# Kernel optimization log

Hardware: AMD Instinct MI355X
Metric: run time of the kernel (lower is better)

The kernel has to match this reference:

```python
import jax, jax.numpy as jnp
import numpy as np

EPS = 1e-5

def _bn(x, g, b):
    # BatchNorm1d in training mode: stats over (batch, length) dims, biased var
    mean = jnp.mean(x, axis=(0, 2), keepdims=True)
    var = jnp.var(x, axis=(0, 2), keepdims=True)
    return (x - mean) * jax.lax.rsqrt(var + EPS) * g[None, :, None] + b[None, :, None]

def _conv1x1(x, w, b):
    # pointwise Conv1d: [B,C,T] x [O,C] -> [B,O,T]
    return jnp.einsum('bct,oc->bot', x, w) + b[None, :, None]

def setup_inputs() -> dict:
    key = jax.random.key(0)
    ks = jax.random.split(key, 4)
    B, C, T = 32, 1024, 2048
    x = jax.random.normal(ks[0], (B, C, T), dtype=jnp.float32)
    w1 = jax.random.normal(ks[1], (256, 1024), dtype=jnp.float32) * (1.0 / np.sqrt(1024))
    w2 = jax.random.normal(ks[2], (64, 256), dtype=jnp.float32) * (1.0 / np.sqrt(256))
    return {
        'x': x,
        'bn1_g': jnp.ones((1024,), jnp.float32), 'bn1_b': jnp.zeros((1024,), jnp.float32),
        'w1': w1, 'b1': jnp.zeros((256,), jnp.float32),
        'bn2_g': jnp.ones((256,), jnp.float32), 'bn2_b': jnp.zeros((256,), jnp.float32),
        'w2': w2, 'b2': jnp.zeros((64,), jnp.float32),
    }

def reference(x, bn1_g, bn1_b, w1, b1, bn2_g, bn2_b, w2, b2):
    # reduction layer: BN -> 1x1 conv -> ReLU (1024 -> 256)
    h = jax.nn.relu(_conv1x1(_bn(x, bn1_g, bn1_b), w1, b1))
    # out layer: BN -> 1x1 conv, no activation (256 -> 64)
    out = _conv1x1(_bn(h, bn2_g, bn2_b), w2, b2)
    o = out.shape[1]
    mu = out[:, : o // 2, :]
    logvar = out[:, o // 2 :, :]
    return (mu, logvar)
```

## Files before the change

kernel.cpp:

```cpp
#include <hip/hip_runtime.h>

#define B_  32
#define C1  1024
#define C2  256
#define T_  2048
#define EPSF 1e-5f
#define BPITCH 40

typedef __attribute__((ext_vector_type(8))) short bf16x8;
typedef __attribute__((ext_vector_type(4))) float f32x4;

static __device__ __forceinline__ unsigned short f2bf(float f) {
    union { float f; unsigned u; } v; v.f = f;
    unsigned r = v.u + 0x7fffu + ((v.u >> 16) & 1u);
    return (unsigned short)(r >> 16);
}
static __device__ __forceinline__ void g2l16(const void* g, void* l) {
    __builtin_amdgcn_global_load_lds(
        (const __attribute__((address_space(1))) unsigned int*)g,
        (__attribute__((address_space(3))) unsigned int*)l, 16, 0, 0);
}

__global__ __launch_bounds__(256) void k_stats(const float* __restrict__ x,
        float* __restrict__ psum, float* __restrict__ psq) {
    int ct = blockIdx.x, b = blockIdx.y, tid = threadIdx.x;
    int c0 = ct * 64;
    int cl = tid >> 2, t4 = tid & 3;
    const float* xrow = x + (size_t)b * C1 * T_ + (size_t)(c0 + cl) * T_ + t4 * 4;
    float s = 0.f, sq = 0.f;
    #pragma unroll 4
    for (int t0 = 0; t0 < T_; t0 += 16) {
        float4 v = *(const float4*)(xrow + t0);
        s  += v.x + v.y + v.z + v.w;
        sq += v.x * v.x + v.y * v.y + v.z * v.z + v.w * v.w;
    }
    s  += __shfl_xor(s, 1);  s  += __shfl_xor(s, 2);
    sq += __shfl_xor(sq, 1); sq += __shfl_xor(sq, 2);
    if (t4 == 0) {
        psum[(size_t)b * C1 + c0 + cl] = s;
        psq [(size_t)b * C1 + c0 + cl] = sq;
    }
}

__global__ __launch_bounds__(256) void k_bnstat1(const float* __restrict__ psum,
        const float* __restrict__ psq, const float* __restrict__ g1,
        const float* __restrict__ bb1, float* __restrict__ sc1, float* __restrict__ sh1) {
    int c = blockIdx.x * 256 + threadIdx.x;
    float s = 0.f, q = 0.f;
    for (int b = 0; b < B_; ++b) {
        s += psum[(size_t)b * C1 + c];
        q += psq[(size_t)b * C1 + c];
    }
    const float n = (float)(B_ * T_);
    float m = s / n;
    float sc = g1[c] * rsqrtf(q / n - m * m + EPSF);
    sc1[c] = sc;
    sh1[c] = bb1[c] - m * sc;
}

__global__ __launch_bounds__(256) void k_fold1(const float* __restrict__ w1,
        const float* __restrict__ b1, const float* __restrict__ sc1,
        const float* __restrict__ sh1, unsigned short* __restrict__ w1e,
        float* __restrict__ b1e) {
    int o = blockIdx.x, tid = threadIdx.x;
    int c = tid * 4;
    float4 w  = ((const float4*)(w1 + (size_t)o * C1))[tid];
    float4 sc = *(const float4*)(sc1 + c);
    float4 sh = *(const float4*)(sh1 + c);
    float p = w.x * sh.x + w.y * sh.y + w.z * sh.z + w.w * sh.w;
    uint2 pk;
    pk.x = (unsigned)f2bf(w.x * sc.x) | ((unsigned)f2bf(w.y * sc.y) << 16);
    pk.y = (unsigned)f2bf(w.z * sc.z) | ((unsigned)f2bf(w.w * sc.w) << 16);
    *((uint2*)(w1e + (size_t)o * C1 + c)) = pk;
    int wave = tid >> 6, lane = tid & 63;
    for (int m = 1; m < 64; m <<= 1) p += __shfl_xor(p, m);
    __shared__ float rs[4];
    if (lane == 0) rs[wave] = p;
    __syncthreads();
    if (tid == 0) b1e[o] = b1[o] + rs[0] + rs[1] + rs[2] + rs[3];
}

__global__ __launch_bounds__(256, 2) void k_gemm1(const float* __restrict__ x,
        const unsigned short* __restrict__ w1e, const float* __restrict__ b1e,
        unsigned short* __restrict__ hT, float* __restrict__ p2s, float* __restrict__ p2q) {
    __shared__ alignas(16) unsigned short sA[2][256 * 32];
    __shared__ alignas(16) unsigned short sB[2][128 * BPITCH];
    int bn = blockIdx.x, b = blockIdx.y;
    int tid = threadIdx.x;
    int wave = tid >> 6, lane = tid & 63;
    int wm = wave >> 1, wn = wave & 1;
    int l15 = lane & 15, q = lane >> 4;
    f32x4 acc[8][4] = {};

    int kk = tid >> 3, tc = tid & 7;
    const float* xbase = x + (size_t)b * C1 * T_ + (size_t)kk * T_ + (size_t)bn * 128 + tc * 4;

    auto stageA = [&](int buf, int k0) {
        #pragma unroll
        for (int i = 0; i < 4; ++i) {
            int idx = (wave * 4 + i) * 64 + lane;
            int row = idx >> 2, cq = idx & 3;
            g2l16(w1e + (size_t)row * C1 + k0 + cq * 8, &sA[buf][(wave * 4 + i) * 512]);
        }
    };
    float4 rB[4];
    auto loadB = [&](int k0) {
        #pragma unroll
        for (int j = 0; j < 4; ++j)
            rB[j] = *(const float4*)(xbase + (size_t)k0 * T_ + j * 32);
    };
    auto writeB = [&](int buf) {
        #pragma unroll
        for (int j = 0; j < 4; ++j) {
            int t = tc * 4 + j * 32;
            unsigned short* p = &sB[buf][t * BPITCH + kk];
            p[0 * BPITCH] = f2bf(rB[j].x);
            p[1 * BPITCH] = f2bf(rB[j].y);
            p[2 * BPITCH] = f2bf(rB[j].z);
            p[3 * BPITCH] = f2bf(rB[j].w);
        }
    };

    loadB(0);
    stageA(0, 0);
    writeB(0);
    __syncthreads();
    int cur = 0;
    for (int kt = 0; kt < 32; ++kt) {
        int nxt = cur ^ 1;
        if (kt < 31) {
            loadB((kt + 1) * 32);
            stageA(nxt, (kt + 1) * 32);
        }
        bf16x8 bfr[4];
        #pragma unroll
        for (int ni = 0; ni < 4; ++ni)
            bfr[ni] = *((const bf16x8*)&sB[cur][(wn * 64 + ni * 16 + l15) * BPITCH + q * 8]);
        #pragma unroll
        for (int mi = 0; mi < 8; ++mi) {
            bf16x8 af = *((const bf16x8*)&sA[cur][(wm * 128 + mi * 16 + l15) * 32 + q * 8]);
            #pragma unroll
            for (int ni = 0; ni < 4; ++ni)
                acc[mi][ni] = __builtin_amdgcn_mfma_f32_16x16x32_bf16(af, bfr[ni], acc[mi][ni], 0, 0, 0);
        }
        if (kt < 31) writeB(nxt);
        __syncthreads();
        cur = nxt;
    }
    int obase = wm * 128;
    int tbase = bn * 128 + wn * 64;
    int prow = (b * 16 + bn) * 2 + wn;
    #pragma unroll
    for (int mi = 0; mi < 8; ++mi) {
        int og = obase + mi * 16 + q * 4;
        float4 bias = *(const float4*)&b1e[og];
        float s0 = 0, s1 = 0, s2 = 0, s3 = 0, q0 = 0, q1 = 0, q2 = 0, q3 = 0;
        #pragma unroll
        for (int ni = 0; ni < 4; ++ni) {
            int t = tbase + ni * 16 + l15;
            float v0 = fmaxf(acc[mi][ni][0] + bias.x, 0.f);
            float v1 = fmaxf(acc[mi][ni][1] + bias.y, 0.f);
            float v2 = fmaxf(acc[mi][ni][2] + bias.z, 0.f);
            float v3 = fmaxf(acc[mi][ni][3] + bias.w, 0.f);
            s0 += v0; q0 += v0 * v0;  s1 += v1; q1 += v1 * v1;
            s2 += v2; q2 += v2 * v2;  s3 += v3; q3 += v3 * v3;
            uint2 pk;
            pk.x = (unsigned)f2bf(v0) | ((unsigned)f2bf(v1) << 16);
            pk.y = (unsigned)f2bf(v2) | ((unsigned)f2bf(v3) << 16);
            *(uint2*)&hT[((size_t)b * T_ + t) * C2 + og] = pk;
        }
        #pragma unroll
        for (int m = 1; m <= 8; m <<= 1) {
            s0 += __shfl_xor(s0, m); s1 += __shfl_xor(s1, m);
            s2 += __shfl_xor(s2, m); s3 += __shfl_xor(s3, m);
            q0 += __shfl_xor(q0, m); q1 += __shfl_xor(q1, m);
            q2 += __shfl_xor(q2, m); q3 += __shfl_xor(q3, m);
        }
        if (l15 == 0) {
            p2s[(size_t)(og + 0) * 1024 + prow] = s0;
            p2s[(size_t)(og + 1) * 1024 + prow] = s1;
            p2s[(size_t)(og + 2) * 1024 + prow] = s2;
            p2s[(size_t)(og + 3) * 1024 + prow] = s3;
            p2q[(size_t)(og + 0) * 1024 + prow] = q0;
            p2q[(size_t)(og + 1) * 1024 + prow] = q1;
            p2q[(size_t)(og + 2) * 1024 + prow] = q2;
            p2q[(size_t)(og + 3) * 1024 + prow] = q3;
        }
    }
}

__global__ __launch_bounds__(256) void k_bnstat2(const float* __restrict__ p2s,
        const float* __restrict__ p2q, const float* __restrict__ g2,
        const float* __restrict__ bb2, float* __restrict__ sc2, float* __restrict__ sh2) {
    int c = blockIdx.x, tid = threadIdx.x;
    float4 a  = *(const float4*)(p2s + (size_t)c * 1024 + tid * 4);
    float4 qv = *(const float4*)(p2q + (size_t)c * 1024 + tid * 4);
    float s = a.x + a.y + a.z + a.w;
    float q = qv.x + qv.y + qv.z + qv.w;
    for (int m = 1; m < 64; m <<= 1) { s += __shfl_xor(s, m); q += __shfl_xor(q, m); }
    __shared__ float rs[4], rq[4];
    int wave = tid >> 6, lane = tid & 63;
    if (lane == 0) { rs[wave] = s; rq[wave] = q; }
    __syncthreads();
    if (tid == 0) {
        s = rs[0] + rs[1] + rs[2] + rs[3];
        q = rq[0] + rq[1] + rq[2] + rq[3];
        const float n = (float)(B_ * T_);
        float m0 = s / n;
        float sc = g2[c] * rsqrtf(q / n - m0 * m0 + EPSF);
        sc2[c] = sc;
        sh2[c] = bb2[c] - m0 * sc;
    }
}

__global__ __launch_bounds__(256) void k_fold2(const float* __restrict__ w2,
        const float* __restrict__ b2, const float* __restrict__ sc2,
        const float* __restrict__ sh2, unsigned short* __restrict__ w2e,
        float* __restrict__ b2e) {
    int o = blockIdx.x, tid = threadIdx.x;
    float w = w2[(size_t)o * C2 + tid];
    w2e[(size_t)o * C2 + tid] = f2bf(w * sc2[tid]);
    float p = w * sh2[tid];
    int wave = tid >> 6, lane = tid & 63;
    for (int m = 1; m < 64; m <<= 1) p += __shfl_xor(p, m);
    __shared__ float rs[4];
    if (lane == 0) rs[wave] = p;
    __syncthreads();
    if (tid == 0) b2e[o] = b2[o] + rs[0] + rs[1] + rs[2] + rs[3];
}

__global__ __launch_bounds__(256) void k_gemm2(const unsigned short* __restrict__ hT,
        const unsigned short* __restrict__ w2e, const float* __restrict__ b2e,
        float* __restrict__ out) {
    __shared__ alignas(16) unsigned short sA[64 * 32];
    __shared__ alignas(16) unsigned short sB[128 * 32];
    int bn = blockIdx.x, b = blockIdx.y;
    int tid = threadIdx.x;
    int wave = tid >> 6, lane = tid & 63;
    int l15 = lane & 15, q = lane >> 4;
    f32x4 acc[4][2] = {};
    const unsigned short* hblk = hT + ((size_t)b * T_ + (size_t)bn * 128) * C2;

    for (int k0 = 0; k0 < C2; k0 += 32) {
        {
            int idx = wave * 64 + lane;
            int row = idx >> 2, cq = idx & 3;
            g2l16(w2e + (size_t)row * C2 + k0 + cq * 8, &sA[wave * 512]);
        }
        #pragma unroll
        for (int i = 0; i < 2; ++i) {
            int idx = (wave * 2 + i) * 64 + lane;
            int row = idx >> 2, cq = idx & 3;
            g2l16(hblk + (size_t)row * C2 + k0 + cq * 8, &sB[(wave * 2 + i) * 512]);
        }
        __syncthreads();
        bf16x8 af[4], bfr[2];
        #pragma unroll
        for (int mi = 0; mi < 4; ++mi)
            af[mi] = *((const bf16x8*)&sA[(mi * 16 + l15) * 32 + q * 8]);
        #pragma unroll
        for (int ni = 0; ni < 2; ++ni)
            bfr[ni] = *((const bf16x8*)&sB[(wave * 32 + ni * 16 + l15) * 32 + q * 8]);
        #pragma unroll
        for (int mi = 0; mi < 4; ++mi)
            #pragma unroll
            for (int ni = 0; ni < 2; ++ni)
                acc[mi][ni] = __builtin_amdgcn_mfma_f32_16x16x32_bf16(af[mi], bfr[ni], acc[mi][ni], 0, 0, 0);
        __syncthreads();
    }
    int tbase = bn * 128 + wave * 32;
    #pragma unroll
    for (int mi = 0; mi < 4; ++mi) {
        #pragma unroll
        for (int reg = 0; reg < 4; ++reg) {
            int o = mi * 16 + q * 4 + reg;
            float bias = b2e[o];
            size_t base = (o < 32)
                ? ((size_t)b * 32 * T_ + (size_t)o * T_)
                : (2097152u + (size_t)b * 32 * T_ + (size_t)(o - 32) * T_);
            #pragma unroll
            for (int ni = 0; ni < 2; ++ni) {
                int t = tbase + ni * 16 + l15;
                out[base + t] = acc[mi][ni][reg] + bias;
            }
        }
    }
}

extern "C" void kernel_launch(void* const* d_in, const int* in_sizes, int n_in,
                              void* d_out, int out_size, void* d_ws, size_t ws_size,
                              hipStream_t stream) {
    const float* x   = (const float*)d_in[0];
    const float* g1  = (const float*)d_in[1];
    const float* bb1 = (const float*)d_in[2];
    const float* w1  = (const float*)d_in[3];
    const float* b1  = (const float*)d_in[4];
    const float* g2  = (const float*)d_in[5];
    const float* bb2 = (const float*)d_in[6];
    const float* w2  = (const float*)d_in[7];
    const float* b2  = (const float*)d_in[8];
    float* out = (float*)d_out;

    char* ws = (char*)d_ws;
    float* b1e  = (float*)(ws + 0);
    float* b2e  = (float*)(ws + 4096);
    float* psum = (float*)(ws + 8192);
    float* psq  = (float*)(ws + 139264);
    float* p2s  = (float*)(ws + 270336);
    float* p2q  = (float*)(ws + 1318912);
    unsigned short* w1e = (unsigned short*)(ws + 2367488);
    unsigned short* w2e = (unsigned short*)(ws + 2891776);
    float* sc1 = (float*)(ws + 2924544);
    float* sh1 = (float*)(ws + 2928640);
    float* sc2 = (float*)(ws + 2932736);
    float* sh2 = (float*)(ws + 2933760);
    unsigned short* hT  = (unsigned short*)(ws + 2934784);

    k_stats  <<<dim3(16, 32), dim3(256), 0, stream>>>(x, psum, psq);
    k_bnstat1<<<dim3(4),      dim3(256), 0, stream>>>(psum, psq, g1, bb1, sc1, sh1);
    k_fold1  <<<dim3(256),    dim3(256), 0, stream>>>(w1, b1, sc1, sh1, w1e, b1e);
    k_gemm1  <<<dim3(16, 32), dim3(256), 0, stream>>>(x, w1e, b1e, hT, p2s, p2q);
    k_bnstat2<<<dim3(256),    dim3(256), 0, stream>>>(p2s, p2q, g2, bb2, sc2, sh2);
    k_fold2  <<<dim3(64),     dim3(256), 0, stream>>>(w2, b2, sc2, sh2, w2e, b2e);
    k_gemm2  <<<dim3(16, 32), dim3(256), 0, stream>>>(hT, w2e, b2e, out);
}
```

Before: 485.1 us.

## Fuse BN stat and fold kernels, swizzle gemm1 B tile, double-buffer gemm2

Merges the BN statistics reduction into the weight-fold kernels, dropping two launches and the intermediate scale/shift buffers. The second fold now accumulates the folded bias with atomics into b2e, which is initialized in the first fold kernel. It also XOR-swizzles the LDS layout of the gemm1 B tile to reduce bank conflicts and double-buffers the gemm2 K loop so loads overlap MFMA work. Risks include atomic ordering nondeterminism in the bias and every fold block redundantly re-reducing the 32-batch partial sums.

```diff
diff --git a/kernel.cpp b/kernel.cpp
--- a/kernel.cpp
+++ b/kernel.cpp
@@ -19,6 +19,9 @@
     __builtin_amdgcn_global_load_lds(
         (const __attribute__((address_space(1))) unsigned int*)g,
         (__attribute__((address_space(3))) unsigned int*)l, 16, 0, 0);
+}
+static __device__ __forceinline__ int bswz(int t) {
+    return ((t >> 2) & 3) ^ ((t >> 4) & 1);
 }
 
 __global__ __launch_bounds__(256) void k_stats(const float* __restrict__ x,
@@ -42,42 +45,45 @@
     }
 }
 
-__global__ __launch_bounds__(256) void k_bnstat1(const float* __restrict__ psum,
-        const float* __restrict__ psq, const float* __restrict__ g1,
-        const float* __restrict__ bb1, float* __restrict__ sc1, float* __restrict__ sh1) {
-    int c = blockIdx.x * 256 + threadIdx.x;
-    float s = 0.f, q = 0.f;
-    for (int b = 0; b < B_; ++b) {
-        s += psum[(size_t)b * C1 + c];
-        q += psq[(size_t)b * C1 + c];
-    }
-    const float n = (float)(B_ * T_);
-    float m = s / n;
-    float sc = g1[c] * rsqrtf(q / n - m * m + EPSF);
-    sc1[c] = sc;
-    sh1[c] = bb1[c] - m * sc;
-}
-
-__global__ __launch_bounds__(256) void k_fold1(const float* __restrict__ w1,
-        const float* __restrict__ b1, const float* __restrict__ sc1,
-        const float* __restrict__ sh1, unsigned short* __restrict__ w1e,
-        float* __restrict__ b1e) {
+__global__ __launch_bounds__(256) void k_bnfold1(const float* __restrict__ w1,
+        const float* __restrict__ b1, const float* __restrict__ g1,
+        const float* __restrict__ bb1, const float* __restrict__ psum,
+        const float* __restrict__ psq, unsigned short* __restrict__ w1e,
+        float* __restrict__ b1e, const float* __restrict__ b2, float* __restrict__ b2e) {
     int o = blockIdx.x, tid = threadIdx.x;
     int c = tid * 4;
-    float4 w  = ((const float4*)(w1 + (size_t)o * C1))[tid];
-    float4 sc = *(const float4*)(sc1 + c);
-    float4 sh = *(const float4*)(sh1 + c);
-    float p = w.x * sh.x + w.y * sh.y + w.z * sh.z + w.w * sh.w;
+    float4 s = {0,0,0,0}, sq = {0,0,0,0};
+    for (int b = 0; b < B_; ++b) {
+        float4 a = *(const float4*)(psum + (size_t)b * C1 + c);
+        float4 q = *(const float4*)(psq  + (size_t)b * C1 + c);
+        s.x += a.x; s.y += a.y; s.z += a.z; s.w += a.w;
+        sq.x += q.x; sq.y += q.y; sq.z += q.z; sq.w += q.w;
+    }
+    const float n = (float)(B_ * T_);
+    float4 gg = *(const float4*)(g1 + c);
+    float4 bv = *(const float4*)(bb1 + c);
+    float m0 = s.x / n, m1 = s.y / n, m2 = s.z / n, m3 = s.w / n;
+    float sc0 = gg.x * rsqrtf(sq.x / n - m0 * m0 + EPSF);
+    float sc1 = gg.y * rsqrtf(sq.y / n - m1 * m1 + EPSF);
+    float sc2 = gg.z * rsqrtf(sq.z / n - m2 * m2 + EPSF);
+    float sc3 = gg.w * rsqrtf(sq.w / n - m3 * m3 + EPSF);
+    float sh0 = bv.x - m0 * sc0, sh1 = bv.y - m1 * sc1;
+    float sh2 = bv.z - m2 * sc2, sh3 = bv.w - m3 * sc3;
+    float4 w = ((const float4*)(w1 + (size_t)o * C1))[tid];
+    float p = w.x * sh0 + w.y * sh1 + w.z * sh2 + w.w * sh3;
     uint2 pk;
-    pk.x = (unsigned)f2bf(w.x * sc.x) | ((unsigned)f2bf(w.y * sc.y) << 16);
-    pk.y = (unsigned)f2bf(w.z * sc.z) | ((unsigned)f2bf(w.w * sc.w) << 16);
+    pk.x = (unsigned)f2bf(w.x * sc0) | ((unsigned)f2bf(w.y * sc1) << 16);
+    pk.y = (unsigned)f2bf(w.z * sc2) | ((unsigned)f2bf(w.w * sc3) << 16);
     *((uint2*)(w1e + (size_t)o * C1 + c)) = pk;
     int wave = tid >> 6, lane = tid & 63;
     for (int m = 1; m < 64; m <<= 1) p += __shfl_xor(p, m);
     __shared__ float rs[4];
     if (lane == 0) rs[wave] = p;
     __syncthreads();
-    if (tid == 0) b1e[o] = b1[o] + rs[0] + rs[1] + rs[2] + rs[3];
+    if (tid == 0) {
+        b1e[o] = b1[o] + rs[0] + rs[1] + rs[2] + rs[3];
+        if (o < 64) b2e[o] = b2[o];
+    }
 }
 
 __global__ __launch_bounds__(256, 2) void k_gemm1(const float* __restrict__ x,
@@ -113,7 +119,8 @@
         #pragma unroll
         for (int j = 0; j < 4; ++j) {
             int t = tc * 4 + j * 32;
-            unsigned short* p = &sB[buf][t * BPITCH + kk];
+            int slot = kk ^ (bswz(t) << 3);
+            unsigned short* p = &sB[buf][t * BPITCH + slot];
             p[0 * BPITCH] = f2bf(rB[j].x);
             p[1 * BPITCH] = f2bf(rB[j].y);
             p[2 * BPITCH] = f2bf(rB[j].z);
@@ -134,8 +141,10 @@
         }
         bf16x8 bfr[4];
         #pragma unroll
-        for (int ni = 0; ni < 4; ++ni)
-            bfr[ni] = *((const bf16x8*)&sB[cur][(wn * 64 + ni * 16 + l15) * BPITCH + q * 8]);
+        for (int ni = 0; ni < 4; ++ni) {
+            int t = wn * 64 + ni * 16 + l15;
+            bfr[ni] = *((const bf16x8*)&sB[cur][t * BPITCH + ((q ^ bswz(t)) << 3)]);
+        }
         #pragma unroll
         for (int mi = 0; mi < 8; ++mi) {
             bf16x8 af = *((const bf16x8*)&sA[cur][(wm * 128 + mi * 16 + l15) * 32 + q * 8]);
@@ -189,16 +198,17 @@
     }
 }
 
-__global__ __launch_bounds__(256) void k_bnstat2(const float* __restrict__ p2s,
+__global__ __launch_bounds__(256) void k_bnfold2(const float* __restrict__ p2s,
         const float* __restrict__ p2q, const float* __restrict__ g2,
-        const float* __restrict__ bb2, float* __restrict__ sc2, float* __restrict__ sh2) {
+        const float* __restrict__ bb2, const float* __restrict__ w2,
+        unsigned short* __restrict__ w2e, float* __restrict__ b2e) {
     int c = blockIdx.x, tid = threadIdx.x;
     float4 a  = *(const float4*)(p2s + (size_t)c * 1024 + tid * 4);
     float4 qv = *(const float4*)(p2q + (size_t)c * 1024 + tid * 4);
     float s = a.x + a.y + a.z + a.w;
     float q = qv.x + qv.y + qv.z + qv.w;
     for (int m = 1; m < 64; m <<= 1) { s += __shfl_xor(s, m); q += __shfl_xor(q, m); }
-    __shared__ float rs[4], rq[4];
+    __shared__ float rs[4], rq[4], bc[2];
     int wave = tid >> 6, lane = tid & 63;
     if (lane == 0) { rs[wave] = s; rq[wave] = q; }
     __syncthreads();
@@ -208,32 +218,22 @@
         const float n = (float)(B_ * T_);
         float m0 = s / n;
         float sc = g2[c] * rsqrtf(q / n - m0 * m0 + EPSF);
-        sc2[c] = sc;
-        sh2[c] = bb2[c] - m0 * sc;
-    }
-}
-
-__global__ __launch_bounds__(256) void k_fold2(const float* __restrict__ w2,
-        const float* __restrict__ b2, const float* __restrict__ sc2,
-        const float* __restrict__ sh2, unsigned short* __restrict__ w2e,
-        float* __restrict__ b2e) {
-    int o = blockIdx.x, tid = threadIdx.x;
-    float w = w2[(size_t)o * C2 + tid];
-    w2e[(size_t)o * C2 + tid] = f2bf(w * sc2[tid]);
-    float p = w * sh2[tid];
-    int wave = tid >> 6, lane = tid & 63;
-    for (int m = 1; m < 64; m <<= 1) p += __shfl_xor(p, m);
-    __shared__ float rs[4];
-    if (lane == 0) rs[wave] = p;
-    __syncthreads();
-    if (tid == 0) b2e[o] = b2[o] + rs[0] + rs[1] + rs[2] + rs[3];
+        bc[0] = sc;
+        bc[1] = bb2[c] - m0 * sc;
+    }
+    __syncthreads();
+    if (tid < 64) {
+        float wv = w2[(size_t)tid * C2 + c];
+        w2e[(size_t)tid * C2 + c] = f2bf(wv * bc[0]);
+        atomicAdd(&b2e[tid], wv * bc[1]);
+    }
 }
 
 __global__ __launch_bounds__(256) void k_gemm2(const unsigned short* __restrict__ hT,
         const unsigned short* __restrict__ w2e, const float* __restrict__ b2e,
         float* __restrict__ out) {
-    __shared__ alignas(16) unsigned short sA[64 * 32];
-    __shared__ alignas(16) unsigned short sB[128 * 32];
+    __shared__ alignas(16) unsigned short sA[2][64 * 32];
+    __shared__ alignas(16) unsigned short sB[2][128 * 32];
     int bn = blockIdx.x, b = blockIdx.y;
     int tid = threadIdx.x;
     int wave = tid >> 6, lane = tid & 63;
@@ -241,32 +241,39 @@
     f32x4 acc[4][2] = {};
     const unsigned short* hblk = hT + ((size_t)b * T_ + (size_t)bn * 128) * C2;
 
-    for (int k0 = 0; k0 < C2; k0 += 32) {
+    auto stage = [&](int buf, int k0) {
         {
             int idx = wave * 64 + lane;
             int row = idx >> 2, cq = idx & 3;
-            g2l16(w2e + (size_t)row * C2 + k0 + cq * 8, &sA[wave * 512]);
+            g2l16(w2e + (size_t)row * C2 + k0 + cq * 8, &sA[buf][wave * 512]);
         }
         #pragma unroll
         for (int i = 0; i < 2; ++i) {
             int idx = (wave * 2 + i) * 64 + lane;
             int row = idx >> 2, cq = idx & 3;
-            g2l16(hblk + (size_t)row * C2 + k0 + cq * 8, &sB[(wave * 2 + i) * 512]);
-        }
-        __syncthreads();
+            g2l16(hblk + (size_t)row * C2 + k0 + cq * 8, &sB[buf][(wave * 2 + i) * 512]);
+        }
+    };
+
+    stage(0, 0);
+    __syncthreads();
+    int cur = 0;
+    for (int kt = 0; kt < 8; ++kt) {
+        if (kt < 7) stage(cur ^ 1, (kt + 1) * 32);
         bf16x8 af[4], bfr[2];
         #pragma unroll
         for (int mi = 0; mi < 4; ++mi)
-            af[mi] = *((const bf16x8*)&sA[(mi * 16 + l15) * 32 + q * 8]);
+            af[mi] = *((const bf16x8*)&sA[cur][(mi * 16 + l15) * 32 + q * 8]);
         #pragma unroll
         for (int ni = 0; ni < 2; ++ni)
-            bfr[ni] = *((const bf16x8*)&sB[(wave * 32 + ni * 16 + l15) * 32 + q * 8]);
+            bfr[ni] = *((const bf16x8*)&sB[cur][(wave * 32 + ni * 16 + l15) * 32 + q * 8]);
         #pragma unroll
         for (int mi = 0; mi < 4; ++mi)
             #pragma unroll
             for (int ni = 0; ni < 2; ++ni)
                 acc[mi][ni] = __builtin_amdgcn_mfma_f32_16x16x32_bf16(af[mi], bfr[ni], acc[mi][ni], 0, 0, 0);
         __syncthreads();
+        cur ^= 1;
     }
     int tbase = bn * 128 + wave * 32;
     #pragma unroll
@@ -310,17 +317,11 @@
     float* p2q  = (float*)(ws + 1318912);
     unsigned short* w1e = (unsigned short*)(ws + 2367488);
     unsigned short* w2e = (unsigned short*)(ws + 2891776);
-    float* sc1 = (float*)(ws + 2924544);
-    float* sh1 = (float*)(ws + 2928640);
-    float* sc2 = (float*)(ws + 2932736);
-    float* sh2 = (float*)(ws + 2933760);
-    unsigned short* hT  = (unsigned short*)(ws + 2934784);
+    unsigned short* hT  = (unsigned short*)(ws + 2924544);
 
     k_stats  <<<dim3(16, 32), dim3(256), 0, stream>>>(x, psum, psq);
-    k_bnstat1<<<dim3(4),      dim3(256), 0, stream>>>(psum, psq, g1, bb1, sc1, sh1);
-    k_fold1  <<<dim3(256),    dim3(256), 0, stream>>>(w1, b1, sc1, sh1, w1e, b1e);
+    k_bnfold1<<<dim3(256),    dim3(256), 0, stream>>>(w1, b1, g1, bb1, psum, psq, w1e, b1e, b2, b2e);
     k_gemm1  <<<dim3(16, 32), dim3(256), 0, stream>>>(x, w1e, b1e, hT, p2s, p2q);
-    k_bnstat2<<<dim3(256),    dim3(256), 0, stream>>>(p2s, p2q, g2, bb2, sc2, sh2);
-    k_fold2  <<<dim3(64),     dim3(256), 0, stream>>>(w2, b2, sc2, sh2, w2e, b2e);
+    k_bnfold2<<<dim3(256),    dim3(256), 0, stream>>>(p2s, p2q, g2, bb2, w2, w2e, b2e);
     k_gemm2  <<<dim3(16, 32), dim3(256), 0, stream>>>(hT, w2e, b2e, out);
 }
```

Result: no change. 492.6 us (+1.6%).
